# Kernel optimization log

Measured on AMD Instinct MI355X. Metric: run time of the kernel, lower is better.

The kernel has to match this reference:

```python
import jax, jax.numpy as jnp
import numpy as np

B, L, DIM, H, HD = 1, 2048, 2048, 16, 128  # head_dim = DIM // H; RoPE pairs = HD // 2


def setup_inputs() -> dict:
    key = jax.random.key(0)
    ks = jax.random.split(key, 6)
    x = jax.random.normal(ks[0], (B, L, DIM), dtype=jnp.float32)
    pe = jax.random.normal(ks[1], (1, 1, L, HD // 2, 2, 2), dtype=jnp.float32)
    qkv_w = jax.random.normal(ks[2], (3 * DIM, DIM), dtype=jnp.float32) * 0.02
    q_scale = jnp.ones((HD,), dtype=jnp.float32)
    k_scale = jnp.ones((HD,), dtype=jnp.float32)
    proj_w = jax.random.normal(ks[3], (DIM, DIM), dtype=jnp.float32) * 0.02
    proj_b = jnp.zeros((DIM,), dtype=jnp.float32)
    return {"x": x, "pe": pe, "qkv_w": qkv_w, "q_scale": q_scale,
            "k_scale": k_scale, "proj_w": proj_w, "proj_b": proj_b}


def _rmsnorm(t, scale):
    # per-head-dim RMSNorm, eps=1e-6, computed in fp32 (inputs already fp32)
    rrms = jax.lax.rsqrt(jnp.mean(t * t, axis=-1, keepdims=True) + 1e-6)
    return t * rrms * scale


def _apply_rope(q, k, pe):
    def rot(t):
        t_ = t.reshape(*t.shape[:-1], -1, 1, 2)  # [B,H,L,HD/2,1,2]
        out = pe[..., 0] * t_[..., 0] + pe[..., 1] * t_[..., 1]  # [B,H,L,HD/2,2]
        return out.reshape(t.shape)
    return rot(q), rot(k)


def reference(x, pe, qkv_w, q_scale, k_scale, proj_w, proj_b):
    b, l, _ = x.shape
    qkv = jnp.einsum('bld,ed->ble', x, qkv_w)  # [B, L, 3*DIM]
    qkv = qkv.reshape(b, l, 3, H, HD)
    # 'B L (K H D) -> K B H L D'
    qkv = jnp.transpose(qkv, (2, 0, 3, 1, 4))
    q, k, v = qkv[0], qkv[1], qkv[2]  # each [B, H, L, HD]
    q = _rmsnorm(q, q_scale)
    k = _rmsnorm(k, k_scale)
    q, k = _apply_rope(q, k, pe)
    scale = 1.0 / jnp.sqrt(jnp.asarray(HD, dtype=q.dtype))
    scores = jnp.einsum('bhqd,bhkd->bhqk', q, k) * scale
    attn = jax.nn.softmax(scores, axis=-1)
    out = jnp.einsum('bhqk,bhkd->bhqd', attn, v)  # [B, H, L, HD]
    out = jnp.transpose(out, (0, 2, 1, 3)).reshape(b, l, H * HD)  # 'B H L D -> B L (H D)'
    return jnp.einsum('bld,ed->ble', out, proj_w) + proj_b
```

## Files before the change

### kernel.cpp

```cpp
#include <hip/hip_runtime.h>
#include <hip/hip_bf16.h>
#include <math.h>

#define L_SEQ 2048
#define DIM   2048
#define NH    16
#define HD    128
#define TDIM  6144

typedef __attribute__((ext_vector_type(8))) short short8;
typedef __attribute__((ext_vector_type(4))) float f32x4;
typedef __attribute__((ext_vector_type(16))) float f32x16;
typedef __attribute__((ext_vector_type(4))) unsigned int u32x4;

__device__ __forceinline__ void gl_lds16(const void* g, void* l) {
  __builtin_amdgcn_global_load_lds(
      (const __attribute__((address_space(1))) unsigned int*)g,
      (__attribute__((address_space(3))) unsigned int*)l, 16, 0, 0);
}

__device__ __forceinline__ short bf16bits(float x) {
  __hip_bfloat16 h = __float2bfloat16(x);
  return *(short*)&h;
}

__device__ __forceinline__ float bits2f(short s) {
  unsigned int u = ((unsigned int)(unsigned short)s) << 16;
  return __uint_as_float(u);
}

__device__ __forceinline__ unsigned int pack_bf16(float a, float b) {
  __hip_bfloat162 h = __float22bfloat162_rn(make_float2(a, b));
  return *(unsigned int*)&h;
}

__global__ __launch_bounds__(256)
void cast3_bf16(const float* __restrict__ a, __hip_bfloat16* __restrict__ oa,
                const float* __restrict__ b, __hip_bfloat16* __restrict__ ob,
                const float* __restrict__ c, __hip_bfloat16* __restrict__ oc) {
  int i = (blockIdx.x * 256 + threadIdx.x) * 8;
  const float* src;
  __hip_bfloat16* dst;
  int off;
  if (i < DIM * DIM)                  { src = a; dst = oa; off = i; }
  else if (i < DIM * DIM + TDIM * DIM){ src = b; dst = ob; off = i - DIM * DIM; }
  else                                { src = c; dst = oc; off = i - DIM * DIM - TDIM * DIM; }
  float4 v0 = *(const float4*)(src + off);
  float4 v1 = *(const float4*)(src + off + 4);
  short8 o;
  o[0] = bf16bits(v0.x); o[1] = bf16bits(v0.y); o[2] = bf16bits(v0.z); o[3] = bf16bits(v0.w);
  o[4] = bf16bits(v1.x); o[5] = bf16bits(v1.y); o[6] = bf16bits(v1.z); o[7] = bf16bits(v1.w);
  *(short8*)(dst + off) = o;
}

#define QKV_N 6144
#define QKV_K 2048

__global__ __launch_bounds__(512, 2)
void gemm_qkv_256(const __hip_bfloat16* __restrict__ A,
                  const __hip_bfloat16* __restrict__ B,
                  __hip_bfloat16* __restrict__ C) {
  extern __shared__ char smem[];
  const int tid  = threadIdx.x;
  const int lane = tid & 63, w = tid >> 6;
  const int l15  = lane & 15, quad = lane >> 4;
  const int wm   = w >> 2, wn = w & 3;

  const int orig = blockIdx.x;
  const int c   = orig & 7;
  const int idx = orig >> 3;
  const int by  = (c >> 2) * 4 + (idx >> 3);
  const int bx  = (c & 3) * 8 + (idx & 7);
  const int m0 = by * 256, n0 = bx * 192;

  const int ar0 = tid >> 2,         aq0 = (tid & 3) ^ ((ar0 >> 1) & 3);
  const int ar1 = (512 + tid) >> 2, aq1 = (tid & 3) ^ ((ar1 >> 1) & 3);
  const __hip_bfloat16* pA0 = A + (size_t)(m0 + ar0) * QKV_K + aq0 * 8;
  const __hip_bfloat16* pA1 = A + (size_t)(m0 + ar1) * QKV_K + aq1 * 8;
  const __hip_bfloat16* pB0 = B + (size_t)(n0 + ar0) * QKV_K + aq0 * 8;
  const __hip_bfloat16* pB1 = B + (size_t)(n0 + ar1) * QKV_K + aq1 * 8;
  const int dst0 = w * 1024;

  f32x4 acc[8][3];
#pragma unroll
  for (int mi = 0; mi < 8; ++mi)
#pragma unroll
    for (int ni = 0; ni < 3; ++ni) acc[mi][ni] = (f32x4){0.f, 0.f, 0.f, 0.f};

  const int sq   = (l15 >> 1) & 3;
  const int aoff = ((wm * 128 + l15) * 32 + (quad ^ sq) * 8) * 2;
  const int boff = 16384 + ((wn * 48 + l15) * 32 + (quad ^ sq) * 8) * 2;

#pragma unroll
  for (int p = 0; p < 3; ++p) {
    char* Sp = smem + p * 28672;
    gl_lds16(pA0 + p * 32, Sp + dst0);
    gl_lds16(pA1 + p * 32, Sp + dst0 + 8192);
    gl_lds16(pB0 + p * 32, Sp + 16384 + dst0);
    if (w < 4) gl_lds16(pB1 + p * 32, Sp + 24576 + dst0);
  }
  if (w < 4) asm volatile("s_waitcnt vmcnt(8)" ::: "memory");
  else       asm volatile("s_waitcnt vmcnt(6)" ::: "memory");
  __builtin_amdgcn_s_barrier();

  for (int tb = 0; tb < 64; tb += 4) {
#pragma unroll
    for (int u = 0; u < 4; ++u) {
      const int t  = tb + u;
      const char* As = smem + (u & 3) * 28672;
      const char* Bs = As;
      const int tn = (t + 3) & 63;
      char* Sn = smem + ((u + 3) & 3) * 28672;

      short8 a[8];
#pragma unroll
      for (int mi = 0; mi < 8; ++mi)
        a[mi] = *(const short8*)(As + aoff + mi * 1024);
      short8 b0 = *(const short8*)(Bs + boff);
      short8 b1 = *(const short8*)(Bs + boff + 1024);
      gl_lds16(pA0 + tn * 32, Sn + dst0);
      gl_lds16(pA1 + tn * 32, Sn + dst0 + 8192);
      __builtin_amdgcn_s_barrier();
      __builtin_amdgcn_s_setprio(1);
#pragma unroll
      for (int mi = 0; mi < 8; ++mi) {
        acc[mi][0] = __builtin_amdgcn_mfma_f32_16x16x32_bf16(a[mi], b0, acc[mi][0], 0, 0, 0);
        acc[mi][1] = __builtin_amdgcn_mfma_f32_16x16x32_bf16(a[mi], b1, acc[mi][1], 0, 0, 0);
      }
      __builtin_amdgcn_s_setprio(0);
      __builtin_amdgcn_s_barrier();

      short8 b2 = *(const short8*)(Bs + boff + 2048);
      gl_lds16(pB0 + tn * 32, Sn + 16384 + dst0);
      if (w < 4) {
        gl_lds16(pB1 + tn * 32, Sn + 24576 + dst0);
        asm volatile("s_waitcnt vmcnt(8)" ::: "memory");
      } else {
        asm volatile("s_waitcnt vmcnt(6)" ::: "memory");
      }
      __builtin_amdgcn_s_barrier();
      __builtin_amdgcn_s_setprio(1);
#pragma unroll
      for (int mi = 0; mi < 8; ++mi)
        acc[mi][2] = __builtin_amdgcn_mfma_f32_16x16x32_bf16(a[mi], b2, acc[mi][2], 0, 0, 0);
      __builtin_amdgcn_s_setprio(0);
      __builtin_amdgcn_s_barrier();
    }
  }

  const int crow = m0 + wm * 128 + quad * 4;
  const int ccol = n0 + wn * 48 + l15;
#pragma unroll
  for (int mi = 0; mi < 8; ++mi)
#pragma unroll
    for (int ni = 0; ni < 3; ++ni)
#pragma unroll
      for (int r = 0; r < 4; ++r)
        C[(size_t)(crow + mi * 16 + r) * QKV_N + ccol + ni * 16] =
            __float2bfloat16(acc[mi][ni][r]);
}

__global__ __launch_bounds__(256)
void qkv_epilogue(const __hip_bfloat16* __restrict__ C,
                  const float* __restrict__ q_scale, const float* __restrict__ k_scale,
                  const float* __restrict__ pe,
                  __hip_bfloat16* __restrict__ Qb, __hip_bfloat16* __restrict__ Kb,
                  __hip_bfloat16* __restrict__ Vt) {
  const int bid = blockIdx.x;
  const int t = threadIdx.x;
  if (bid < 512) {
    const int sec = bid >> 8;
    const int h   = (bid >> 4) & 15;
    const int rb  = bid & 15;
    const float* scale = sec ? k_scale : q_scale;
    const float qmul = sec ? 1.0f : 0.08838834764831845f;
    __hip_bfloat16* dst = sec ? Kb : Qb;

    const int row = t >> 1, half = t & 1;
    const int l = rb * 128 + row;
    const __hip_bfloat16* grow = C + (size_t)l * TDIM + sec * DIM + h * HD + half * 64;

    float ss = 0.f;
#pragma unroll
    for (int c8 = 0; c8 < 64; c8 += 8) {
      short8 v8 = *(const short8*)(grow + c8);
#pragma unroll
      for (int j = 0; j < 8; ++j) { float f = bits2f(v8[j]); ss += f * f; }
    }
    ss += __shfl_xor(ss, 1);
    const float rrms = rsqrtf(ss * (1.f / 128.f) + 1e-6f);

    const float* perow = pe + (size_t)l * 256 + half * 128;
    __hip_bfloat16* drow = dst + ((size_t)h * L_SEQ + l) * HD + half * 64;

#pragma unroll
    for (int c8 = 0; c8 < 64; c8 += 8) {
      short8 v8 = *(const short8*)(grow + c8);
      float f[8];
#pragma unroll
      for (int j = 0; j < 8; ++j)
        f[j] = bits2f(v8[j]) * rrms * scale[half * 64 + c8 + j];
      short8 o;
#pragma unroll
      for (int p = 0; p < 4; ++p) {
        float4 pp = *(const float4*)(perow + c8 * 2 + p * 4);
        float e = f[2 * p], od = f[2 * p + 1];
        o[2 * p]     = bf16bits((pp.x * e + pp.y * od) * qmul);
        o[2 * p + 1] = bf16bits((pp.z * e + pp.w * od) * qmul);
      }
      *(short8*)(drow + c8) = o;
    }
  } else {
    __shared__ short Tt[128 * 72];
    const int vb = bid - 512;
    const int h = vb >> 5, lb = vb & 31;
    const int l0 = lb * 64;
#pragma unroll
    for (int k = 0; k < 4; ++k) {
      int idx = t + k * 256;
      int row = idx >> 4, c = idx & 15;
      short8 v = *(const short8*)(C + (size_t)(l0 + row) * TDIM + 2 * DIM + h * HD + c * 8);
#pragma unroll
      for (int j = 0; j < 8; ++j) Tt[(c * 8 + j) * 72 + row] = v[j];
    }
    __syncthreads();
    const int d = t >> 1, lh = t & 1;
    __hip_bfloat16* vrow = Vt + ((size_t)h * HD + d) * L_SEQ + l0 + lh * 32;
#pragma unroll
    for (int k = 0; k < 4; ++k) {
      short8 o = *(const short8*)&Tt[d * 72 + lh * 32 + k * 8];
      *(short8*)(vrow + k * 8) = o;
    }
  }
}

#define PJ_N 2048
#define PJ_K 2048

__global__ __launch_bounds__(256, 2)
void gemm_proj_128(const __hip_bfloat16* __restrict__ A,
                   const __hip_bfloat16* __restrict__ B,
                   const float* __restrict__ bias, float* __restrict__ C) {
  __shared__ __align__(16) char smem[65536];
  const int tid  = threadIdx.x;
  const int lane = tid & 63, w = tid >> 6;
  const int l15  = lane & 15, quad = lane >> 4;
  const int wm   = (w >> 1) * 64, wn = (w & 1) * 64;

  const int orig = blockIdx.x;
  const int c   = orig & 7;
  const int idx = orig >> 3;
  const int by  = (c >> 1) * 4 + (idx & 3);
  const int bx  = (c & 1) * 8 + (idx >> 2);
  const int m0 = by * 128, n0 = bx * 128;

  const int ar0 = tid >> 2,         aq0 = (tid & 3) ^ ((ar0 >> 1) & 3);
  const int ar1 = (256 + tid) >> 2, aq1 = (tid & 3) ^ ((ar1 >> 1) & 3);
  const __hip_bfloat16* pA0 = A + (size_t)(m0 + ar0) * PJ_K + aq0 * 8;
  const __hip_bfloat16* pA1 = A + (size_t)(m0 + ar1) * PJ_K + aq1 * 8;
  const __hip_bfloat16* pB0 = B + (size_t)(n0 + ar0) * PJ_K + aq0 * 8;
  const __hip_bfloat16* pB1 = B + (size_t)(n0 + ar1) * PJ_K + aq1 * 8;
  const int dst0 = w * 1024;

  f32x4 acc[4][4];
#pragma unroll
  for (int mi = 0; mi < 4; ++mi)
#pragma unroll
    for (int ni = 0; ni < 4; ++ni) acc[mi][ni] = (f32x4){0.f, 0.f, 0.f, 0.f};

  const int sq   = (l15 >> 1) & 3;
  const int aoff = ((wm + l15) * 32 + (quad ^ sq) * 8) * 2;
  const int boff = 8192 + ((wn + l15) * 32 + (quad ^ sq) * 8) * 2;

#pragma unroll
  for (int p = 0; p < 3; ++p) {
    char* Sp = smem + p * 16384;
    gl_lds16(pA0 + p * 32, Sp + dst0);
    gl_lds16(pA1 + p * 32, Sp + dst0 + 4096);
    gl_lds16(pB0 + p * 32, Sp + 8192 + dst0);
    gl_lds16(pB1 + p * 32, Sp + 8192 + dst0 + 4096);
  }
  asm volatile("s_waitcnt vmcnt(8)\n\ts_barrier" ::: "memory");

  for (int tb = 0; tb < 64; tb += 4) {
#pragma unroll
    for (int u = 0; u < 4; ++u) {
      const int t  = tb + u;
      const char* As = smem + u * 16384;
      const char* Bs = As;
      const int tn = (t + 3) & 63;
      char* Sn = smem + ((u + 3) & 3) * 16384;

      short8 a[4];
#pragma unroll
      for (int mi = 0; mi < 4; ++mi)
        a[mi] = *(const short8*)(As + aoff + mi * 1024);
      short8 b0 = *(const short8*)(Bs + boff);
      short8 b1 = *(const short8*)(Bs + boff + 1024);
      gl_lds16(pA0 + tn * 32, Sn + dst0);
      gl_lds16(pA1 + tn * 32, Sn + dst0 + 4096);
      __builtin_amdgcn_s_barrier();
      __builtin_amdgcn_s_setprio(1);
#pragma unroll
      for (int mi = 0; mi < 4; ++mi) {
        acc[mi][0] = __builtin_amdgcn_mfma_f32_16x16x32_bf16(a[mi], b0, acc[mi][0], 0, 0, 0);
        acc[mi][1] = __builtin_amdgcn_mfma_f32_16x16x32_bf16(a[mi], b1, acc[mi][1], 0, 0, 0);
      }
      __builtin_amdgcn_s_setprio(0);
      __builtin_amdgcn_s_barrier();

      short8 b2 = *(const short8*)(Bs + boff + 2048);
      short8 b3 = *(const short8*)(Bs + boff + 3072);
      gl_lds16(pB0 + tn * 32, Sn + 8192 + dst0);
      gl_lds16(pB1 + tn * 32, Sn + 8192 + dst0 + 4096);
      asm volatile("s_waitcnt vmcnt(8)\n\ts_barrier" ::: "memory");
      __builtin_amdgcn_s_setprio(1);
#pragma unroll
      for (int mi = 0; mi < 4; ++mi) {
        acc[mi][2] = __builtin_amdgcn_mfma_f32_16x16x32_bf16(a[mi], b2, acc[mi][2], 0, 0, 0);
        acc[mi][3] = __builtin_amdgcn_mfma_f32_16x16x32_bf16(a[mi], b3, acc[mi][3], 0, 0, 0);
      }
      __builtin_amdgcn_s_setprio(0);
      __builtin_amdgcn_s_barrier();
    }
  }

  const int crow = m0 + wm + quad * 4;
  const int ccol = n0 + wn + l15;
#pragma unroll
  for (int mi = 0; mi < 4; ++mi)
#pragma unroll
    for (int ni = 0; ni < 4; ++ni) {
      float bv = bias[ccol + ni * 16];
#pragma unroll
      for (int r = 0; r < 4; ++r)
        C[(size_t)(crow + mi * 16 + r) * PJ_N + ccol + ni * 16] =
            acc[mi][ni][r] + bv;
    }
}

#define NZ 4
#define ZLEN (L_SEQ / NZ)

__global__ __launch_bounds__(256, 3)
void attn_mfma(const __hip_bfloat16* __restrict__ Qb,
               const __hip_bfloat16* __restrict__ Kb,
               const __hip_bfloat16* __restrict__ Vt,
               __hip_bfloat16* __restrict__ Opart, float2* __restrict__ ml) {
  const int orig = blockIdx.x;
  const int wg   = (orig & 7) * 128 + (orig >> 3);
  const int h    = wg >> 6;
  const int rem  = wg & 63;
  const int z    = rem >> 4;
  const int q0   = (rem & 15) * 128;
  const int t    = threadIdx.x;
  const int lane = t & 63, w = t >> 6;
  const int l31  = lane & 31;
  const int u    = lane >> 5;

  __shared__ __align__(16) __hip_bfloat16 Ks[64 * 128];
  __shared__ __align__(16) __hip_bfloat16 Vs[128 * 64];

  const __hip_bfloat16* kbase = Kb + (size_t)h * L_SEQ * HD;
  const __hip_bfloat16* vbase = Vt + (size_t)h * HD * L_SEQ;

  short8 aq[8];
  {
    const __hip_bfloat16* qb = Qb + ((size_t)h * L_SEQ + q0 + w * 32 + l31) * HD + u * 8;
#pragma unroll
    for (int hh = 0; hh < 8; ++hh)
      aq[hh] = *(const short8*)(qb + hh * 16);
  }

  f32x16 o[4];
#pragma unroll
  for (int dt = 0; dt < 4; ++dt)
#pragma unroll
    for (int r = 0; r < 16; ++r) o[dt][r] = 0.f;
  float m_run = -1e30f, l_run = 0.f;

  for (int kt = 0; kt < ZLEN / 64; ++kt) {
    const int k0 = z * ZLEN + kt * 64;
#pragma unroll
    for (int i = 0; i < 4; ++i) {
      int krow = w * 16 + i * 4 + (lane >> 4);
      int kch  = (lane & 15) ^ (krow & 7);
      gl_lds16(kbase + (size_t)(k0 + krow) * HD + kch * 8,
               &Ks[(w * 16 + i * 4) * 128]);
    }
#pragma unroll
    for (int i = 0; i < 4; ++i) {
      int vrow = w * 32 + i * 8 + (lane >> 3);
      int vch  = (lane & 7) ^ (vrow & 7);
      gl_lds16(vbase + (size_t)vrow * L_SEQ + k0 + vch * 8,
               &Vs[(w * 32 + i * 8) * 64]);
    }
    __syncthreads();

#pragma unroll
    for (int ks = 0; ks < 2; ++ks) {
      const int krow = ks * 32 + l31;
      const char* krowp = (const char*)Ks + krow * 256;
      const int ksw = krow & 7;
      f32x16 s;
#pragma unroll
      for (int r = 0; r < 16; ++r) s[r] = 0.f;
      __builtin_amdgcn_s_setprio(1);
#pragma unroll
      for (int hh = 0; hh < 8; ++hh) {
        short8 ak = *(const short8*)(krowp + ((hh * 2 + u) ^ ksw) * 16);
        s = __builtin_amdgcn_mfma_f32_32x32x16_bf16(ak, aq[hh], s, 0, 0, 0);
      }
      __builtin_amdgcn_s_setprio(0);

      float rm = s[0];
#pragma unroll
      for (int r = 1; r < 16; ++r) rm = fmaxf(rm, s[r]);
      rm = fmaxf(rm, __shfl_xor(rm, 32));

      if (!__all(rm <= m_run + 8.f)) {
        float mnew = fmaxf(m_run, rm);
        float alpha = __expf(m_run - mnew);
        m_run = mnew;
        l_run *= alpha;
#pragma unroll
        for (int dt = 0; dt < 4; ++dt)
#pragma unroll
          for (int r = 0; r < 16; ++r) o[dt][r] *= alpha;
      }

      float sum = 0.f;
#pragma unroll
      for (int r = 0; r < 16; ++r) {
        float p = __expf(s[r] - m_run);
        s[r] = p;
        sum += p;
      }
      sum += __shfl_xor(sum, 32);
      l_run += sum;

      unsigned int W0 = pack_bf16(s[0],  s[1]),  W1 = pack_bf16(s[2],  s[3]);
      unsigned int W2 = pack_bf16(s[4],  s[5]),  W3 = pack_bf16(s[6],  s[7]);
      unsigned int W4 = pack_bf16(s[8],  s[9]),  W5 = pack_bf16(s[10], s[11]);
      unsigned int W6 = pack_bf16(s[12], s[13]), W7 = pack_bf16(s[14], s[15]);
      asm("v_permlane32_swap_b32 %0, %1" : "+v"(W0), "+v"(W2));
      asm("v_permlane32_swap_b32 %0, %1" : "+v"(W1), "+v"(W3));
      asm("v_permlane32_swap_b32 %0, %1" : "+v"(W4), "+v"(W6));
      asm("v_permlane32_swap_b32 %0, %1" : "+v"(W5), "+v"(W7));
      u32x4 pb0 = {W0, W1, W2, W3};
      u32x4 pb1 = {W4, W5, W6, W7};
      short8 ap0 = *(short8*)&pb0;
      short8 ap1 = *(short8*)&pb1;

      __builtin_amdgcn_s_setprio(1);
#pragma unroll
      for (int dt = 0; dt < 4; ++dt) {
        const int d = dt * 32 + l31;
        const char* vrowp = (const char*)Vs + d * 128;
        const int vsw = d & 7;
        short8 av0 = *(const short8*)(vrowp + ((ks * 4 + u) ^ vsw) * 16);
        o[dt] = __builtin_amdgcn_mfma_f32_32x32x16_bf16(av0, ap0, o[dt], 0, 0, 0);
        short8 av1 = *(const short8*)(vrowp + ((ks * 4 + 2 + u) ^ vsw) * 16);
        o[dt] = __builtin_amdgcn_mfma_f32_32x32x16_bf16(av1, ap1, o[dt], 0, 0, 0);
      }
      __builtin_amdgcn_s_setprio(0);
    }
    __syncthreads();
  }

  const float linv = 1.f / l_run;
  char* Ot = (char*)Ks + w * 8192;
  const int qsw = l31 & 7;
#pragma unroll
  for (int dt = 0; dt < 4; ++dt)
#pragma unroll
    for (int p = 0; p < 8; ++p) {
      unsigned int v = pack_bf16(o[dt][2 * p] * linv, o[dt][2 * p + 1] * linv);
      int dpair = dt * 16 + (p & 1) + (p >> 1) * 4 + 2 * u;
      *(unsigned int*)(Ot + l31 * 256 + ((dpair >> 2) ^ qsw) * 16 + (dpair & 3) * 4) = v;
    }
  __syncthreads();
  {
    const int qr = lane >> 1, half = lane & 1;
    const char* Orow = (char*)Ks + w * 8192 + qr * 256;
    __hip_bfloat16* gout =
        Opart + ((size_t)(z * NH + h) * L_SEQ + q0 + w * 32 + qr) * HD;
#pragma unroll
    for (int c8 = 0; c8 < 8; ++c8) {
      int chunk = half * 8 + c8;
      short8 v = *(const short8*)(Orow + ((chunk ^ (qr & 7)) * 16));
      *(short8*)(gout + chunk * 8) = v;
    }
  }
  if (lane < 32) {
    size_t rb = (size_t)(z * NH + h) * L_SEQ + q0 + w * 32;
    ml[rb + l31] = make_float2(m_run, l_run);
  }
}

__global__ __launch_bounds__(256)
void attn_combine4(const __hip_bfloat16* __restrict__ Opart,
                   const float2* __restrict__ ml,
                   __hip_bfloat16* __restrict__ out) {
  const int h  = blockIdx.y;
  const int q  = blockIdx.x * 16 + (threadIdx.x >> 4);
  const int d8 = (threadIdx.x & 15) * 8;
  size_t idx[NZ];
  float2 a[NZ];
#pragma unroll
  for (int zz = 0; zz < NZ; ++zz) {
    idx[zz] = ((size_t)zz * NH + h) * L_SEQ + q;
    a[zz] = ml[idx[zz]];
  }
  float M = fmaxf(fmaxf(a[0].x, a[1].x), fmaxf(a[2].x, a[3].x));
  float wz[NZ];
  float tot = 0.f;
#pragma unroll
  for (int zz = 0; zz < NZ; ++zz) {
    wz[zz] = __expf(a[zz].x - M) * a[zz].y;
    tot += wz[zz];
  }
  float inv = 1.f / tot;
  float acc[8] = {0.f, 0.f, 0.f, 0.f, 0.f, 0.f, 0.f, 0.f};
#pragma unroll
  for (int zz = 0; zz < NZ; ++zz) {
    short8 ov = *(const short8*)&Opart[idx[zz] * HD + d8];
#pragma unroll
    for (int j = 0; j < 8; ++j) acc[j] += wz[zz] * bits2f(ov[j]);
  }
  short8 r;
#pragma unroll
  for (int j = 0; j < 8; ++j) r[j] = bf16bits(acc[j] * inv);
  *(short8*)&out[(size_t)q * DIM + h * HD + d8] = r;
}

extern "C" void kernel_launch(void* const* d_in, const int* in_sizes, int n_in,
                              void* d_out, int out_size, void* d_ws, size_t ws_size,
                              hipStream_t stream) {
  const float* x       = (const float*)d_in[0];
  const float* pe      = (const float*)d_in[1];
  const float* qkv_w   = (const float*)d_in[2];
  const float* q_scale = (const float*)d_in[3];
  const float* k_scale = (const float*)d_in[4];
  const float* proj_w  = (const float*)d_in[5];
  const float* proj_b  = (const float*)d_in[6];
  float* out = (float*)d_out;

  char* base = (char*)d_ws;
  __hip_bfloat16* xb       = (__hip_bfloat16*)base;
  __hip_bfloat16* wb       = (__hip_bfloat16*)(base + 8388608);
  __hip_bfloat16* Cq       = (__hip_bfloat16*)(base + 33554432);
  __hip_bfloat16* pwb      = (__hip_bfloat16*)(base + 58720256);
  __hip_bfloat16* Qb       = (__hip_bfloat16*)base;
  __hip_bfloat16* Kb       = (__hip_bfloat16*)(base + 8388608);
  __hip_bfloat16* Vt       = (__hip_bfloat16*)(base + 16777216);
  __hip_bfloat16* Opart    = (__hip_bfloat16*)(base + 25165824);
  float2*         ml       = (float2*)d_out;
  __hip_bfloat16* attn_out = (__hip_bfloat16*)base;

  static bool attr_done = false;
  if (!attr_done) {
    hipFuncSetAttribute((const void*)gemm_qkv_256,
                        hipFuncAttributeMaxDynamicSharedMemorySize, 131072);
    attr_done = true;
  }

  cast3_bf16<<<dim3((2 * DIM * DIM + TDIM * DIM) / (256 * 8)), 256, 0, stream>>>(
      x, xb, qkv_w, wb, proj_w, pwb);

  gemm_qkv_256<<<dim3(256), 512, 114688, stream>>>(xb, wb, Cq);

  qkv_epilogue<<<dim3(1024), 256, 0, stream>>>(Cq, q_scale, k_scale, pe, Qb, Kb, Vt);

  attn_mfma<<<dim3(NZ * NH * (L_SEQ / 128)), 256, 0, stream>>>(Qb, Kb, Vt, Opart, ml);

  attn_combine4<<<dim3(L_SEQ / 16, NH), 256, 0, stream>>>(Opart, ml, attn_out);

  gemm_proj_128<<<dim3(256), 256, 0, stream>>>(attn_out, pwb, proj_b, out);
}
```

Baseline: 281.1 us.

## Double-buffer K/V tiles in attention kernel with 32-key stages

```diff
diff --git a/kernel.cpp b/kernel.cpp
--- a/kernel.cpp
+++ b/kernel.cpp
@@ -358,11 +358,30 @@
   const int l31  = lane & 31;
   const int u    = lane >> 5;
 
-  __shared__ __align__(16) __hip_bfloat16 Ks[64 * 128];
-  __shared__ __align__(16) __hip_bfloat16 Vs[128 * 64];
+  __shared__ __align__(16) char smem[32768];
+  __hip_bfloat16* Ks = (__hip_bfloat16*)smem;
+  __hip_bfloat16* Vs = (__hip_bfloat16*)(smem + 16384);
 
   const __hip_bfloat16* kbase = Kb + (size_t)h * L_SEQ * HD;
   const __hip_bfloat16* vbase = Vt + (size_t)h * HD * L_SEQ;
+
+  auto STAGE = [&](int kt_, int b_) {
+    const int k0_ = z * ZLEN + kt_ * 32;
+#pragma unroll
+    for (int i = 0; i < 2; ++i) {
+      int krow = w * 8 + i * 4 + (lane >> 4);
+      int kch  = (lane & 15) ^ (krow & 7);
+      gl_lds16(kbase + (size_t)(k0_ + krow) * HD + kch * 8,
+               Ks + b_ * 4096 + (w * 8 + i * 4) * 128);
+    }
+#pragma unroll
+    for (int i = 0; i < 2; ++i) {
+      int vrow = w * 32 + i * 16 + (lane >> 2);
+      int vch  = (lane & 3) ^ (vrow & 3);
+      gl_lds16(vbase + (size_t)vrow * L_SEQ + k0_ + vch * 8,
+               Vs + b_ * 4096 + (w * 32 + i * 16) * 32);
+    }
+  };
 
   short8 aq[8];
   {
@@ -379,97 +398,89 @@
     for (int r = 0; r < 16; ++r) o[dt][r] = 0.f;
   float m_run = -1e30f, l_run = 0.f;
 
-  for (int kt = 0; kt < ZLEN / 64; ++kt) {
-    const int k0 = z * ZLEN + kt * 64;
-#pragma unroll
-    for (int i = 0; i < 4; ++i) {
-      int krow = w * 16 + i * 4 + (lane >> 4);
-      int kch  = (lane & 15) ^ (krow & 7);
-      gl_lds16(kbase + (size_t)(k0 + krow) * HD + kch * 8,
-               &Ks[(w * 16 + i * 4) * 128]);
-    }
-#pragma unroll
-    for (int i = 0; i < 4; ++i) {
-      int vrow = w * 32 + i * 8 + (lane >> 3);
-      int vch  = (lane & 7) ^ (vrow & 7);
-      gl_lds16(vbase + (size_t)vrow * L_SEQ + k0 + vch * 8,
-               &Vs[(w * 32 + i * 8) * 64]);
-    }
-    __syncthreads();
-
-#pragma unroll
-    for (int ks = 0; ks < 2; ++ks) {
-      const int krow = ks * 32 + l31;
-      const char* krowp = (const char*)Ks + krow * 256;
-      const int ksw = krow & 7;
-      f32x16 s;
-#pragma unroll
-      for (int r = 0; r < 16; ++r) s[r] = 0.f;
-      __builtin_amdgcn_s_setprio(1);
-#pragma unroll
-      for (int hh = 0; hh < 8; ++hh) {
-        short8 ak = *(const short8*)(krowp + ((hh * 2 + u) ^ ksw) * 16);
-        s = __builtin_amdgcn_mfma_f32_32x32x16_bf16(ak, aq[hh], s, 0, 0, 0);
-      }
-      __builtin_amdgcn_s_setprio(0);
-
-      float rm = s[0];
-#pragma unroll
-      for (int r = 1; r < 16; ++r) rm = fmaxf(rm, s[r]);
-      rm = fmaxf(rm, __shfl_xor(rm, 32));
-
-      if (!__all(rm <= m_run + 8.f)) {
-        float mnew = fmaxf(m_run, rm);
-        float alpha = __expf(m_run - mnew);
-        m_run = mnew;
-        l_run *= alpha;
-#pragma unroll
-        for (int dt = 0; dt < 4; ++dt)
-#pragma unroll
-          for (int r = 0; r < 16; ++r) o[dt][r] *= alpha;
-      }
-
-      float sum = 0.f;
-#pragma unroll
-      for (int r = 0; r < 16; ++r) {
-        float p = __expf(s[r] - m_run);
-        s[r] = p;
-        sum += p;
-      }
-      sum += __shfl_xor(sum, 32);
-      l_run += sum;
-
-      unsigned int W0 = pack_bf16(s[0],  s[1]),  W1 = pack_bf16(s[2],  s[3]);
-      unsigned int W2 = pack_bf16(s[4],  s[5]),  W3 = pack_bf16(s[6],  s[7]);
-      unsigned int W4 = pack_bf16(s[8],  s[9]),  W5 = pack_bf16(s[10], s[11]);
-      unsigned int W6 = pack_bf16(s[12], s[13]), W7 = pack_bf16(s[14], s[15]);
-      asm("v_permlane32_swap_b32 %0, %1" : "+v"(W0), "+v"(W2));
-      asm("v_permlane32_swap_b32 %0, %1" : "+v"(W1), "+v"(W3));
-      asm("v_permlane32_swap_b32 %0, %1" : "+v"(W4), "+v"(W6));
-      asm("v_permlane32_swap_b32 %0, %1" : "+v"(W5), "+v"(W7));
-      u32x4 pb0 = {W0, W1, W2, W3};
-      u32x4 pb1 = {W4, W5, W6, W7};
-      short8 ap0 = *(short8*)&pb0;
-      short8 ap1 = *(short8*)&pb1;
-
-      __builtin_amdgcn_s_setprio(1);
-#pragma unroll
-      for (int dt = 0; dt < 4; ++dt) {
-        const int d = dt * 32 + l31;
-        const char* vrowp = (const char*)Vs + d * 128;
-        const int vsw = d & 7;
-        short8 av0 = *(const short8*)(vrowp + ((ks * 4 + u) ^ vsw) * 16);
-        o[dt] = __builtin_amdgcn_mfma_f32_32x32x16_bf16(av0, ap0, o[dt], 0, 0, 0);
-        short8 av1 = *(const short8*)(vrowp + ((ks * 4 + 2 + u) ^ vsw) * 16);
-        o[dt] = __builtin_amdgcn_mfma_f32_32x32x16_bf16(av1, ap1, o[dt], 0, 0, 0);
-      }
-      __builtin_amdgcn_s_setprio(0);
-    }
-    __syncthreads();
+  const int NT = ZLEN / 32;
+  STAGE(0, 0);
+  asm volatile("s_waitcnt vmcnt(0)" ::: "memory");
+  __builtin_amdgcn_s_barrier();
+
+  for (int kt = 0; kt < NT; ++kt) {
+    const int buf = kt & 1;
+    if (kt + 1 < NT) STAGE(kt + 1, buf ^ 1);
+
+    const __hip_bfloat16* Kc = Ks + buf * 4096;
+    const __hip_bfloat16* Vc = Vs + buf * 4096;
+
+    const char* krowp = (const char*)(Kc + l31 * 128);
+    const int ksw = l31 & 7;
+    f32x16 s;
+#pragma unroll
+    for (int r = 0; r < 16; ++r) s[r] = 0.f;
+    __builtin_amdgcn_s_setprio(1);
+#pragma unroll
+    for (int hh = 0; hh < 8; ++hh) {
+      short8 ak = *(const short8*)(krowp + ((hh * 2 + u) ^ ksw) * 16);
+      s = __builtin_amdgcn_mfma_f32_32x32x16_bf16(ak, aq[hh], s, 0, 0, 0);
+    }
+    __builtin_amdgcn_s_setprio(0);
+
+    float rm = s[0];
+#pragma unroll
+    for (int r = 1; r < 16; ++r) rm = fmaxf(rm, s[r]);
+    rm = fmaxf(rm, __shfl_xor(rm, 32));
+
+    if (!__all(rm <= m_run + 8.f)) {
+      float mnew = fmaxf(m_run, rm);
+      float alpha = __expf(m_run - mnew);
+      m_run = mnew;
+      l_run *= alpha;
+#pragma unroll
+      for (int dt = 0; dt < 4; ++dt)
+#pragma unroll
+        for (int r = 0; r < 16; ++r) o[dt][r] *= alpha;
+    }
+
+    float sum = 0.f;
+#pragma unroll
+    for (int r = 0; r < 16; ++r) {
+      float p = __expf(s[r] - m_run);
+      s[r] = p;
+      sum += p;
+    }
+    sum += __shfl_xor(sum, 32);
+    l_run += sum;
+
+    unsigned int W0 = pack_bf16(s[0],  s[1]),  W1 = pack_bf16(s[2],  s[3]);
+    unsigned int W2 = pack_bf16(s[4],  s[5]),  W3 = pack_bf16(s[6],  s[7]);
+    unsigned int W4 = pack_bf16(s[8],  s[9]),  W5 = pack_bf16(s[10], s[11]);
+    unsigned int W6 = pack_bf16(s[12], s[13]), W7 = pack_bf16(s[14], s[15]);
+    asm("v_permlane32_swap_b32 %0, %1" : "+v"(W0), "+v"(W2));
+    asm("v_permlane32_swap_b32 %0, %1" : "+v"(W1), "+v"(W3));
+    asm("v_permlane32_swap_b32 %0, %1" : "+v"(W4), "+v"(W6));
+    asm("v_permlane32_swap_b32 %0, %1" : "+v"(W5), "+v"(W7));
+    u32x4 pb0 = {W0, W1, W2, W3};
+    u32x4 pb1 = {W4, W5, W6, W7};
+    short8 ap0 = *(short8*)&pb0;
+    short8 ap1 = *(short8*)&pb1;
+
+    __builtin_amdgcn_s_setprio(1);
+#pragma unroll
+    for (int dt = 0; dt < 4; ++dt) {
+      const int d = dt * 32 + l31;
+      const char* vrowp = (const char*)(Vc + d * 32);
+      const int vsw = d & 3;
+      short8 av0 = *(const short8*)(vrowp + ((u) ^ vsw) * 16);
+      o[dt] = __builtin_amdgcn_mfma_f32_32x32x16_bf16(av0, ap0, o[dt], 0, 0, 0);
+      short8 av1 = *(const short8*)(vrowp + ((2 + u) ^ vsw) * 16);
+      o[dt] = __builtin_amdgcn_mfma_f32_32x32x16_bf16(av1, ap1, o[dt], 0, 0, 0);
+    }
+    __builtin_amdgcn_s_setprio(0);
+
+    asm volatile("s_waitcnt vmcnt(0)" ::: "memory");
+    __builtin_amdgcn_s_barrier();
   }
 
   const float linv = 1.f / l_run;
-  char* Ot = (char*)Ks + w * 8192;
+  char* Ot = smem + w * 8192;
   const int qsw = l31 & 7;
 #pragma unroll
   for (int dt = 0; dt < 4; ++dt)
@@ -482,7 +493,7 @@
   __syncthreads();
   {
     const int qr = lane >> 1, half = lane & 1;
-    const char* Orow = (char*)Ks + w * 8192 + qr * 256;
+    const char* Orow = smem + w * 8192 + qr * 256;
     __hip_bfloat16* gout =
         Opart + ((size_t)(z * NH + h) * L_SEQ + q0 + w * 32 + qr) * HD;
 #pragma unroll
```

New measurement: 287.3 us. 2.2% more time.

## Prefetch next K/V tile: K via registers, V double-buffered in LDS

Applied to the files above, without the earlier changes.

```diff
diff --git a/kernel.cpp b/kernel.cpp
--- a/kernel.cpp
+++ b/kernel.cpp
@@ -358,11 +358,37 @@
   const int l31  = lane & 31;
   const int u    = lane >> 5;
 
-  __shared__ __align__(16) __hip_bfloat16 Ks[64 * 128];
-  __shared__ __align__(16) __hip_bfloat16 Vs[128 * 64];
+  __shared__ __align__(16) char smem[49152];
+  __hip_bfloat16* Ks = (__hip_bfloat16*)smem;
+  __hip_bfloat16* Vs = (__hip_bfloat16*)(smem + 16384);
 
   const __hip_bfloat16* kbase = Kb + (size_t)h * L_SEQ * HD;
   const __hip_bfloat16* vbase = Vt + (size_t)h * HD * L_SEQ;
+
+  auto LOADK = [&](int kt_, u32x4* kr) {
+    const int k0_ = z * ZLEN + kt_ * 64;
+#pragma unroll
+    for (int i = 0; i < 4; ++i) {
+      int krow = w * 16 + i * 4 + (lane >> 4);
+      int kch  = (lane & 15) ^ (krow & 7);
+      kr[i] = *(const u32x4*)(kbase + (size_t)(k0_ + krow) * HD + kch * 8);
+    }
+  };
+  auto WRITEK = [&](u32x4* kr) {
+#pragma unroll
+    for (int i = 0; i < 4; ++i)
+      *(u32x4*)((char*)Ks + (w * 16 + i * 4) * 256 + lane * 16) = kr[i];
+  };
+  auto STAGEV = [&](int kt_, int b_) {
+    const int k0_ = z * ZLEN + kt_ * 64;
+#pragma unroll
+    for (int i = 0; i < 4; ++i) {
+      int vrow = w * 32 + i * 8 + (lane >> 3);
+      int vch  = (lane & 7) ^ (vrow & 7);
+      gl_lds16(vbase + (size_t)vrow * L_SEQ + k0_ + vch * 8,
+               (char*)Vs + b_ * 16384 + (w * 32 + i * 8) * 128);
+    }
+  };
 
   short8 aq[8];
   {
@@ -379,23 +405,18 @@
     for (int r = 0; r < 16; ++r) o[dt][r] = 0.f;
   float m_run = -1e30f, l_run = 0.f;
 
+  u32x4 kr[4];
+  LOADK(0, kr);
+  STAGEV(0, 0);
+  WRITEK(kr);
+  __syncthreads();
+
   for (int kt = 0; kt < ZLEN / 64; ++kt) {
-    const int k0 = z * ZLEN + kt * 64;
-#pragma unroll
-    for (int i = 0; i < 4; ++i) {
-      int krow = w * 16 + i * 4 + (lane >> 4);
-      int kch  = (lane & 15) ^ (krow & 7);
-      gl_lds16(kbase + (size_t)(k0 + krow) * HD + kch * 8,
-               &Ks[(w * 16 + i * 4) * 128]);
-    }
-#pragma unroll
-    for (int i = 0; i < 4; ++i) {
-      int vrow = w * 32 + i * 8 + (lane >> 3);
-      int vch  = (lane & 7) ^ (vrow & 7);
-      gl_lds16(vbase + (size_t)vrow * L_SEQ + k0 + vch * 8,
-               &Vs[(w * 32 + i * 8) * 64]);
-    }
-    __syncthreads();
+    const int buf = kt & 1;
+    if (kt + 1 < ZLEN / 64) {
+      LOADK(kt + 1, kr);
+      STAGEV(kt + 1, buf ^ 1);
+    }
 
 #pragma unroll
     for (int ks = 0; ks < 2; ++ks) {
@@ -456,7 +477,7 @@
 #pragma unroll
       for (int dt = 0; dt < 4; ++dt) {
         const int d = dt * 32 + l31;
-        const char* vrowp = (const char*)Vs + d * 128;
+        const char* vrowp = (const char*)Vs + buf * 16384 + d * 128;
         const int vsw = d & 7;
         short8 av0 = *(const short8*)(vrowp + ((ks * 4 + u) ^ vsw) * 16);
         o[dt] = __builtin_amdgcn_mfma_f32_32x32x16_bf16(av0, ap0, o[dt], 0, 0, 0);
@@ -465,11 +486,14 @@
       }
       __builtin_amdgcn_s_setprio(0);
     }
+
     __syncthreads();
+    if (kt + 1 < ZLEN / 64) WRITEK(kr);
+    __syncthreads();
   }
 
   const float linv = 1.f / l_run;
-  char* Ot = (char*)Ks + w * 8192;
+  char* Ot = smem + w * 8192;
   const int qsw = l31 & 7;
 #pragma unroll
   for (int dt = 0; dt < 4; ++dt)
@@ -482,7 +506,7 @@
   __syncthreads();
   {
     const int qr = lane >> 1, half = lane & 1;
-    const char* Orow = (char*)Ks + w * 8192 + qr * 256;
+    const char* Orow = smem + w * 8192 + qr * 256;
     __hip_bfloat16* gout =
         Opart + ((size_t)(z * NH + h) * L_SEQ + q0 + w * 32 + qr) * HD;
 #pragma unroll
```

New measurement: 300.5 us. 1.07x slower.
